# Kernel optimization log

Measured on AMD Instinct MI355X. Metric: run time of the kernel, lower is better.

## Reference

```python
import jax, jax.numpy as jnp
import numpy as np

H = 1536      # hidden_size
V = 128       # input_size == output_size (char vocab)
ML = 128      # MAX_LENGTH
SOS = 0


def setup_inputs() -> dict:
    key = jax.random.key(0)
    ks = jax.random.split(key, 16)
    s = 1.0 / np.sqrt(H)
    f = lambda k, shp: jax.random.uniform(k, shp, jnp.float32, -s, s)
    return {
        "input_tensor": jax.random.randint(ks[0], (64,), 0, V),
        "max_length": ML,
        # encoder params
        "emb_enc": f(ks[1], (V, H)),
        "enc_Wih": f(ks[2], (3 * H, H)),
        "enc_Whh": f(ks[3], (3 * H, H)),
        "enc_bih": f(ks[4], (3 * H,)),
        "enc_bhh": f(ks[5], (3 * H,)),
        # decoder params
        "emb_dec": f(ks[6], (V, H)),
        "attn_W": f(ks[7], (ML + 1, 2 * H)),
        "attn_b": f(ks[8], (ML + 1,)),
        "comb_W": f(ks[9], (H, 2 * H)),
        "comb_b": f(ks[10], (H,)),
        "dec_Wih": f(ks[11], (3 * H, H)),
        "dec_Whh": f(ks[12], (3 * H, H)),
        "dec_bih": f(ks[13], (3 * H,)),
        "dec_bhh": f(ks[14], (3 * H,)),
        "out_W": f(ks[15], (V, H)),
        "out_b": jnp.zeros((V,), jnp.float32),
    }


def gru_step(x, h, Wih, Whh, bih, bhh):
    # PyTorch GRUCell math
    gi = Wih @ x + bih
    gh = Whh @ h + bhh
    i_r, i_z, i_n = jnp.split(gi, 3)
    h_r, h_z, h_n = jnp.split(gh, 3)
    r = jax.nn.sigmoid(i_r + h_r)
    z = jax.nn.sigmoid(i_z + h_z)
    n = jnp.tanh(i_n + r * h_n)
    return (1.0 - z) * n + z * h


def reference(input_tensor, max_length, emb_enc, enc_Wih, enc_Whh, enc_bih,
              enc_bhh, emb_dec, attn_W, attn_b, comb_W, comb_b, dec_Wih,
              dec_Whh, dec_bih, dec_bhh, out_W, out_b):
    L = input_tensor.shape[0]

    # ---- encoder: sequential GRU over input tokens ----
    def enc_step(h, tok):
        h = gru_step(emb_enc[tok], h, enc_Wih, enc_Whh, enc_bih, enc_bhh)
        return h, h
    h0 = jnp.zeros((H,), emb_enc.dtype)
    enc_h, enc_outs = jax.lax.scan(enc_step, h0, input_tensor)  # (L, H)
    encoder_outputs = jnp.zeros((max_length + 1, H), emb_enc.dtype).at[:L].set(enc_outs)

    # ---- attention decoder: greedy decode for max_length steps ----
    def dec_step(carry, _):
        h, tok = carry
        emb = emb_dec[tok]                                   # (H,)
        attn_logits = attn_W @ jnp.concatenate([emb, h]) + attn_b
        attn_w = jax.nn.softmax(attn_logits)                 # (ML+1,)
        context = attn_w @ encoder_outputs                   # (H,)
        x = jax.nn.relu(comb_W @ jnp.concatenate([emb, context]) + comb_b)
        h = gru_step(x, h, dec_Wih, dec_Whh, dec_bih, dec_bhh)
        logp = jax.nn.log_softmax(out_W @ h + out_b)         # (V,)
        nxt = jnp.argmax(logp).astype(tok.dtype)
        return (h, nxt), (logp, nxt)

    tok0 = jnp.asarray(SOS, input_tensor.dtype)
    _, (logps, tokens) = jax.lax.scan(dec_step, (enc_h, tok0), None,
                                      length=max_length)
    return logps, tokens  # (ML, V) log-probs, (ML,) greedy token ids
```

## Files before the change

### kernel.cpp

```cpp
#include <hip/hip_runtime.h>
#include <math.h>

#define H     1536
#define H3    4608
#define V     128
#define ML    128
#define MLP1  129
#define LEN   64
#define NBLK  256
#define NTHR  384
#define WPB   6
#define NWAVE (NBLK*WPB)
#define ACC_N    260
#define ACC_ROWS 8
#define ACC_STEP (ACC_ROWS*ACC_N)
#define TA_STRIDE 132

#define SCALEF     1099511627776.0f
#define INV_SCALED 9.094947017729282379150390625e-13

#define CH_ENC 0
#define CH_EX  1
#define CH_EH  2
#define CH_EA  3

#define OFF_BAR 0
#define OFF_CNT 4096
#define OFF_ACC 8192
#define MEMSET_BYTES 2154752
#define OFF_HS  2154752
#define OFF_XS  2941184
#define OFF_XE  3727616
#define OFF_GI  4120832
#define OFF_EO  5300480
#define OFF_M   5693696
#define OFF_TA  6086912
#define OFF_TC  6154496
#define OFF_CT  6940928
#define WS_END  8538368

__device__ __forceinline__ void uc_stf(float* p, float v){
  __hip_atomic_store(p, v, __ATOMIC_RELAXED, __HIP_MEMORY_SCOPE_AGENT);
}
__device__ __forceinline__ unsigned uc_ldu(const unsigned* p){
  return __hip_atomic_load(p, __ATOMIC_RELAXED, __HIP_MEMORY_SCOPE_AGENT);
}
__device__ __forceinline__ void uc_stu64(unsigned long long* p, unsigned long long v){
  __hip_atomic_store(p, v, __ATOMIC_RELAXED, __HIP_MEMORY_SCOPE_AGENT);
}

__device__ __forceinline__ void bump(unsigned* cnt, int ch, int b){
  __hip_atomic_fetch_add(cnt + (ch*16 + (b>>4))*16, 1u,
                         __ATOMIC_RELAXED, __HIP_MEMORY_SCOPE_AGENT);
}
__device__ __forceinline__ void waitline(const unsigned* cnt, int ch, int tid,
                                         unsigned target){
  if(tid < 16){
    const unsigned* line = cnt + (ch*16 + tid)*16;
    while(uc_ldu(line) < target) __builtin_amdgcn_s_sleep(1);
  }
}

__device__ __forceinline__ float wred(float v){
  #pragma unroll
  for(int s=32;s>0;s>>=1) v += __shfl_xor(v, s, 64);
  return v;
}

__device__ __forceinline__ void load6(const float* p, int lane, float4 r[6]){
  const float4* q = (const float4*)p;
  #pragma unroll
  for(int c=0;c<6;c++) r[c] = q[c*64+lane];
}
__device__ __forceinline__ float dot4(const float4 a, const float4 b){
  return a.x*b.x + a.y*b.y + a.z*b.z + a.w*b.w;
}
__device__ __forceinline__ float dot6(const float4 a[6], const float4 b[6]){
  float s=0.f;
  #pragma unroll
  for(int c=0;c<6;c++) s += dot4(a[c], b[c]);
  return s;
}

__device__ __forceinline__ void gbar(unsigned* bar, int rnd){
  __syncthreads();
  if(threadIdx.x==0){
    unsigned* grp  = bar + 32*(1 + (blockIdx.x >> 4));
    unsigned* root = bar;
    unsigned a = __hip_atomic_fetch_add(grp, 1u, __ATOMIC_RELAXED, __HIP_MEMORY_SCOPE_AGENT);
    if((a & 0xFFFFu) == (unsigned)(16*rnd + 15)){
      unsigned ra = __hip_atomic_fetch_add(root, 1u, __ATOMIC_RELAXED, __HIP_MEMORY_SCOPE_AGENT);
      if(ra == (unsigned)(16*rnd + 15)){
        #pragma unroll
        for(int g=0; g<16; g++)
          __hip_atomic_fetch_add(bar + 32*(1+g), 0x10000u,
                                 __ATOMIC_RELAXED, __HIP_MEMORY_SCOPE_AGENT);
      } else {
        while((uc_ldu(grp) >> 16) < (unsigned)(rnd+1))
          __builtin_amdgcn_s_sleep(1);
      }
    } else {
      while((uc_ldu(grp) >> 16) < (unsigned)(rnd+1))
        __builtin_amdgcn_s_sleep(1);
    }
  }
  __syncthreads();
}

__global__ __launch_bounds__(NTHR, 2)
void seq2seq_kernel(const int* __restrict__ toks,
                    const float* __restrict__ emb_enc,
                    const float* __restrict__ enc_Wih,
                    const float* __restrict__ enc_Whh,
                    const float* __restrict__ enc_bih,
                    const float* __restrict__ enc_bhh,
                    const float* __restrict__ emb_dec,
                    const float* __restrict__ attn_W,
                    const float* __restrict__ attn_b,
                    const float* __restrict__ comb_W,
                    const float* __restrict__ comb_b,
                    const float* __restrict__ dec_Wih,
                    const float* __restrict__ dec_Whh,
                    const float* __restrict__ dec_bih,
                    const float* __restrict__ dec_bhh,
                    const float* __restrict__ out_W,
                    const float* __restrict__ out_b,
                    float* __restrict__ out,
                    char* __restrict__ ws)
{
  const int tid = threadIdx.x, b = blockIdx.x;
  const int lane = tid & 63, w = tid >> 6;
  const int gw = b*WPB + w;
  int rnd = 0;

  unsigned* bar = (unsigned*)ws;
  unsigned* cnt = (unsigned*)(ws + OFF_CNT);
  unsigned long long* accseq = (unsigned long long*)(ws + OFF_ACC);
  float* hseq = (float*)(ws + OFF_HS);
  float* xseq = (float*)(ws + OFF_XS);
  float* Xe = (float*)(ws + OFF_XE);
  float* Gi = (float*)(ws + OFF_GI);
  float* EO = (float*)(ws + OFF_EO);
  float* Mm = (float*)(ws + OFF_M);
  float* tA = (float*)(ws + OFF_TA);
  float* tC = (float*)(ws + OFF_TC);
  float* cT = (float*)(ws + OFF_CT);

  __shared__ float smem[WPB*3*H];
  __shared__ float sh[H];
  __shared__ float sx[H];
  __shared__ float scT[WPB*ACC_N];
  __shared__ float sv[ACC_N];
  __shared__ float shc[8];

  for(int idx = b*NTHR + tid; idx < LEN*H; idx += NBLK*NTHR){
    int t = idx / H, k = idx - t*H;
    uc_stf(&Xe[idx], emb_enc[toks[t]*H + k]);
  }
  for(int idx = b*NTHR + tid; idx < H*257; idx += NBLK*NTHR){
    int i = idx / 257, c = idx - i*257;
    float v = (c < MLP1) ? attn_W[(size_t)c*2*H + H + i]
                         : out_W[(size_t)(c-MLP1)*H + i];
    uc_stf(&cT[(size_t)i*ACC_N + c], v);
  }
  gbar(bar, rnd++);

  {
    int r = b*18 + w*3;
    for(int g=0; g<4; g++){
      __syncthreads();
      for(int idx = tid; idx < 16*384; idx += NTHR)
        ((float4*)smem)[idx] = ((const float4*)Xe)[g*16*384 + idx];
      __syncthreads();
      float4 rv0[6], rv1[6], rv2[6];
      load6(enc_Wih + (size_t)r*H,     lane, rv0);
      load6(enc_Wih + (size_t)(r+1)*H, lane, rv1);
      load6(enc_Wih + (size_t)(r+2)*H, lane, rv2);
      float a0[16], a1[16], a2[16];
      #pragma unroll
      for(int t2=0;t2<16;t2++){ a0[t2]=0.f; a1[t2]=0.f; a2[t2]=0.f; }
      #pragma unroll
      for(int c=0;c<6;c++){
        #pragma unroll
        for(int t2=0;t2<16;t2++){
          float4 x = ((float4*)smem)[t2*384 + c*64 + lane];
          a0[t2] += dot4(rv0[c], x);
          a1[t2] += dot4(rv1[c], x);
          a2[t2] += dot4(rv2[c], x);
        }
      }
      float bi0 = enc_bih[r], bi1 = enc_bih[r+1], bi2 = enc_bih[r+2];
      #pragma unroll
      for(int t2=0;t2<16;t2++){
        float s0 = wred(a0[t2]), s1 = wred(a1[t2]), s2 = wred(a2[t2]);
        if(lane==0){
          uc_stf(&Gi[(size_t)(g*16+t2)*H3 + r    ], s0 + bi0);
          uc_stf(&Gi[(size_t)(g*16+t2)*H3 + r + 1], s1 + bi1);
          uc_stf(&Gi[(size_t)(g*16+t2)*H3 + r + 2], s2 + bi2);
        }
      }
    }
  }
  gbar(bar, rnd++);

  {
    int i = gw;
    float4 rv[6]; load6(comb_W + (size_t)i*2*H, lane, rv);
    for(int g=0; g<8; g++){
      __syncthreads();
      for(int idx = tid; idx < 16*384; idx += NTHR)
        ((float4*)smem)[idx] = ((const float4*)emb_dec)[g*16*384 + idx];
      __syncthreads();
      float a0[16];
      #pragma unroll
      for(int t2=0;t2<16;t2++) a0[t2]=0.f;
      #pragma unroll
      for(int c=0;c<6;c++){
        #pragma unroll
        for(int t2=0;t2<16;t2++){
          float4 x = ((float4*)smem)[t2*384 + c*64 + lane];
          a0[t2] += dot4(rv[c], x);
        }
      }
      #pragma unroll
      for(int t2=0;t2<16;t2++){
        float s = wred(a0[t2]);
        if(lane==0) uc_stf(&tC[(size_t)(g*16+t2)*H + i], s);
      }
    }
  }

  for(int task = gw; task < MLP1*V; task += NWAVE){
    int j = task >> 7, v = task & 127;
    float4 av[6]; load6(attn_W + (size_t)j*2*H, lane, av);
    float4 ev[6]; load6(emb_dec + (size_t)v*H, lane, ev);
    float s = wred(dot6(av, ev));
    if(lane==0) uc_stf(&tA[v*TA_STRIDE + j], s);
  }
  gbar(bar, rnd++);

  for(int idx = tid; idx < 18*384; idx += NTHR){
    int row = idx/384, k4 = idx - row*384;
    int w2 = row/3, gate = row - w2*3;
    ((float4*)smem)[idx] =
      ((const float4*)enc_Whh)[((size_t)gate*H + b*WPB + w2)*384 + k4];
  }
  const int i0 = gw;
  float gi0 = Gi[(size_t)lane*H3 + i0];
  float gi1 = Gi[(size_t)lane*H3 + i0 + H];
  float gi2 = Gi[(size_t)lane*H3 + i0 + 2*H];
  float eb0 = enc_bhh[i0], eb1 = enc_bhh[i0+H], eb2 = enc_bhh[i0+2*H];
  __syncthreads();

  for(int t=0; t<LEN; t++){
    if(t==0){
      float4 z4 = {0.f,0.f,0.f,0.f};
      ((float4*)sh)[tid] = z4;
    } else {
      waitline(cnt, CH_ENC, tid, (unsigned)(16*t));
      __syncthreads();
      ((float4*)sh)[tid] = ((const float4*)(EO + (size_t)(t-1)*H))[tid];
    }
    __syncthreads();
    float4 hv[6]; load6(sh, lane, hv);
    const float hp = sh[i0];
    float s[3];
    #pragma unroll
    for(int g=0; g<3; g++){
      const float4* sr = (const float4*)smem + (w*3+g)*384;
      float t0=0.f;
      #pragma unroll
      for(int c=0;c<6;c++) t0 += dot4(sr[c*64+lane], hv[c]);
      s[g] = wred(t0);
    }
    float ir = __shfl(gi0, t, 64), iz = __shfl(gi1, t, 64), in_ = __shfl(gi2, t, 64);
    if(lane==0){
      float r = 1.f/(1.f+expf(-(ir + s[0] + eb0)));
      float z = 1.f/(1.f+expf(-(iz + s[1] + eb1)));
      float n = tanhf(in_ + r*(s[2] + eb2));
      float hn = (1.f-z)*n + z*hp;
      uc_stf(&EO[(size_t)t*H + i0], hn);
    }
    __syncthreads();
    if(tid==0) bump(cnt, CH_ENC, b);
  }
  waitline(cnt, CH_ENC, tid, (unsigned)(16*LEN));
  __syncthreads();

  {
    int i = gw;
    float4 rv[6]; load6(comb_W + (size_t)i*2*H + H, lane, rv);
    for(int g=0; g<4; g++){
      __syncthreads();
      for(int idx = tid; idx < 16*384; idx += NTHR)
        ((float4*)smem)[idx] = ((const float4*)EO)[g*16*384 + idx];
      __syncthreads();
      float a0[16];
      #pragma unroll
      for(int t2=0;t2<16;t2++) a0[t2]=0.f;
      #pragma unroll
      for(int c=0;c<6;c++){
        #pragma unroll
        for(int t2=0;t2<16;t2++){
          float4 x = ((float4*)smem)[t2*384 + c*64 + lane];
          a0[t2] += dot4(rv[c], x);
        }
      }
      #pragma unroll
      for(int t2=0;t2<16;t2++){
        float s = wred(a0[t2]);
        if(lane==0) uc_stf(&Mm[(size_t)i*64 + g*16 + t2], s);
      }
    }
  }

  if(gw < MLP1){
    int j = gw;
    float4 av[6]; load6(attn_W + (size_t)j*2*H + H, lane, av);
    float4 hv[6]; load6(EO + (size_t)(LEN-1)*H, lane, hv);
    float s = wred(dot6(av, hv));
    if(lane==0)
      uc_stu64(&accseq[j], (unsigned long long)(long long)rintf(s*SCALEF));
  }
  for(int idx = tid; idx < 18*384; idx += NTHR){
    int row = idx/384, k4 = idx - row*384;
    int w2 = row/3, gate = row - w2*3;
    ((float4*)smem)[idx] =
      ((const float4*)dec_Whh)[((size_t)gate*H + b*WPB + w2)*384 + k4];
  }
  for(int idx = tid; idx < WPB*ACC_N; idx += NTHR){
    int w2 = idx / ACC_N, c = idx - w2*ACC_N;
    scT[idx] = cT[(size_t)(b*WPB + w2)*ACC_N + c];
  }
  gbar(bar, rnd++);

  const int i = gw;
  float4 wx0[6], wx1[6], wx2[6];
  load6(dec_Wih + (size_t)i*H,         lane, wx0);
  load6(dec_Wih + ((size_t)H + i)*H,   lane, wx1);
  load6(dec_Wih + ((size_t)2*H + i)*H, lane, wx2);
  const float mreg = Mm[(size_t)i*64 + lane];
  const float ct0 = tC[(size_t)lane*H + i];
  const float ct1 = tC[(size_t)(64+lane)*H + i];
  const float ib0 = dec_bih[i], ib1 = dec_bih[i+H], ib2 = dec_bih[i+2*H];
  const float hb0 = dec_bhh[i], hb1 = dec_bhh[i+H], hb2 = dec_bhh[i+2*H];
  const float cb  = comb_b[i];
  const float ob0 = out_b[lane], ob1 = out_b[64+lane];
  const float ab0 = attn_b[lane], ab1 = attn_b[64+lane], ab2 = attn_b[128];

  for(int t=0; t<ML; t++){
    const unsigned long long* accC = accseq + (size_t)t*ACC_STEP;
    unsigned long long* accA = accseq + (size_t)(t+1)*ACC_STEP;

    if(t==0){
      ((float4*)sh)[tid] = ((const float4*)(EO + (size_t)(LEN-1)*H))[tid];
    } else {
      waitline(cnt, CH_EH, tid, (unsigned)(16*t));
      __syncthreads();
      ((float4*)sh)[tid] = ((const float4*)(hseq + (size_t)(t-1)*H))[tid];
    }
    __syncthreads();

    float4 hv[6]; load6(sh, lane, hv);
    const float hp = sh[i];
    float sWh[3];
    #pragma unroll
    for(int g=0; g<3; g++){
      const float4* sp = (const float4*)smem + (w*3+g)*384;
      float t1=0.f;
      #pragma unroll
      for(int c=0;c<6;c++) t1 += dot4(sp[c*64+lane], hv[c]);
      sWh[g] = wred(t1);
    }

    if(t>0) waitline(cnt, CH_EA, tid, (unsigned)(16*t));
    __syncthreads();
    if(tid < 257){
      long long s = 0;
      #pragma unroll
      for(int r2=0; r2<ACC_ROWS; r2++)
        s += ((const long long*)accC)[r2*ACC_N + tid];
      sv[tid] = (float)((double)s * INV_SCALED);
    }
    __syncthreads();

    float o0 = sv[MLP1+lane]    + ob0;
    float o1 = sv[MLP1+64+lane] + ob1;
    float mv; int mi;
    if(o0 >= o1){ mv=o0; mi=lane; } else { mv=o1; mi=64+lane; }
    #pragma unroll
    for(int sft=32; sft>0; sft>>=1){
      float ov = __shfl_xor(mv, sft, 64);
      int   oi = __shfl_xor(mi, sft, 64);
      if(ov > mv || (ov == mv && oi < mi)){ mv = ov; mi = oi; }
    }
    const int tok = (t==0) ? 0 : mi;

    float v0 = sv[lane]      + tA[tok*TA_STRIDE + lane]      + ab0;
    float v1 = sv[64+lane]   + tA[tok*TA_STRIDE + 64 + lane] + ab1;
    float v2 = (lane==0) ? (sv[128] + tA[tok*TA_STRIDE + 128] + ab2) : -1e30f;
    float m0 = fmaxf(fmaxf(v0, v1), v2);
    #pragma unroll
    for(int sft=32; sft>0; sft>>=1) m0 = fmaxf(m0, __shfl_xor(m0, sft, 64));
    float e0 = expf(v0 - m0);
    float esum = e0 + expf(v1 - m0) + ((lane==0) ? expf(v2 - m0) : 0.f);
    esum = wred(esum);
    const float invd = 1.f/esum;

    {
      float s = wred(mreg * e0);
      float ctv = (tok < 64) ? __shfl(ct0, tok, 64) : __shfl(ct1, tok-64, 64);
      if(lane==0)
        uc_stf(&xseq[(size_t)t*H + i], fmaxf(ctv + s*invd + cb, 0.f));
    }
    __syncthreads();
    if(tid==0) bump(cnt, CH_EX, b);

    waitline(cnt, CH_EX, tid, (unsigned)(16*(t+1)));
    __syncthreads();
    ((float4*)sx)[tid] = ((const float4*)(xseq + (size_t)t*H))[tid];
    __syncthreads();
    float4 xv[6]; load6(sx, lane, xv);
    float t0=0.f, t1=0.f, t2=0.f;
    #pragma unroll
    for(int c=0;c<6;c++){
      t0 += dot4(wx0[c], xv[c]);
      t1 += dot4(wx1[c], xv[c]);
      t2 += dot4(wx2[c], xv[c]);
    }
    float sWx0 = wred(t0), sWx1 = wred(t1), sWx2 = wred(t2);
    if(lane==0){
      float r = 1.f/(1.f+expf(-(sWx0+ib0 + sWh[0]+hb0)));
      float z = 1.f/(1.f+expf(-(sWx1+ib1 + sWh[1]+hb1)));
      float n = tanhf(sWx2+ib2 + r*(sWh[2]+hb2));
      float hn = (1.f-z)*n + z*hp;
      uc_stf(&hseq[(size_t)t*H + i], hn);
      shc[w] = hn;
    }
    __syncthreads();
    if(tid==0) bump(cnt, CH_EH, b);

    if(tid < 257){
      float s = 0.f;
      #pragma unroll
      for(int w2=0; w2<WPB; w2++)
        s += scT[w2*ACC_N + tid] * shc[w2];
      atomicAdd(&accA[(b & (ACC_ROWS-1))*ACC_N + tid],
                (unsigned long long)(long long)rintf(s*SCALEF));
    }
    __syncthreads();
    if(tid==0) bump(cnt, CH_EA, b);
  }

  waitline(cnt, CH_EA, tid, (unsigned)(16*ML));
  __syncthreads();
  if(b < ML && w == 0){
    const unsigned long long* accC = accseq + (size_t)(b+1)*ACC_STEP;
    long long s0 = 0, s1 = 0;
    #pragma unroll
    for(int r2=0; r2<ACC_ROWS; r2++){
      s0 += ((const long long*)accC)[r2*ACC_N + MLP1 + lane];
      s1 += ((const long long*)accC)[r2*ACC_N + MLP1 + 64 + lane];
    }
    float o0 = (float)((double)s0 * INV_SCALED) + ob0;
    float o1 = (float)((double)s1 * INV_SCALED) + ob1;
    float mv; int mi;
    if(o0 >= o1){ mv=o0; mi=lane; } else { mv=o1; mi=64+lane; }
    #pragma unroll
    for(int sft=32; sft>0; sft>>=1){
      float ov = __shfl_xor(mv, sft, 64);
      int   oi = __shfl_xor(mi, sft, 64);
      if(ov > mv || (ov == mv && oi < mi)){ mv = ov; mi = oi; }
    }
    float e0 = expf(o0-mv) + expf(o1-mv);
    float ss = wred(e0);
    float lse = mv + logf(ss);
    out[(size_t)b*V + lane]      = o0 - lse;
    out[(size_t)b*V + 64 + lane] = o1 - lse;
    if(lane==0) out[(size_t)ML*V + b] = (float)mi;
  }
}

extern "C" void kernel_launch(void* const* d_in, const int* in_sizes, int n_in,
                              void* d_out, int out_size, void* d_ws, size_t ws_size,
                              hipStream_t stream){
  (void)in_sizes; (void)n_in; (void)out_size; (void)ws_size;
  const int*   toks    = (const int*)  d_in[0];
  const float* emb_enc = (const float*)d_in[2];
  const float* enc_Wih = (const float*)d_in[3];
  const float* enc_Whh = (const float*)d_in[4];
  const float* enc_bih = (const float*)d_in[5];
  const float* enc_bhh = (const float*)d_in[6];
  const float* emb_dec = (const float*)d_in[7];
  const float* attn_W  = (const float*)d_in[8];
  const float* attn_b  = (const float*)d_in[9];
  const float* comb_W  = (const float*)d_in[10];
  const float* comb_b  = (const float*)d_in[11];
  const float* dec_Wih = (const float*)d_in[12];
  const float* dec_Whh = (const float*)d_in[13];
  const float* dec_bih = (const float*)d_in[14];
  const float* dec_bhh = (const float*)d_in[15];
  const float* out_W   = (const float*)d_in[16];
  const float* out_b   = (const float*)d_in[17];
  float* outp = (float*)d_out;
  char*  ws   = (char*)d_ws;

  hipMemsetAsync(d_ws, 0, MEMSET_BYTES, stream);

  void* args[] = { &toks, &emb_enc, &enc_Wih, &enc_Whh, &enc_bih, &enc_bhh,
                   &emb_dec, &attn_W, &attn_b, &comb_W, &comb_b,
                   &dec_Wih, &dec_Whh, &dec_bih, &dec_bhh, &out_W, &out_b,
                   &outp, &ws };
  hipLaunchCooperativeKernel((void*)seq2seq_kernel, dim3(NBLK), dim3(NTHR),
                             args, 0, stream);
}
```

Measured before the change: 2.040 ms.

## Spread arrival counters over more lines and drop LDS staging of shared vectors

Counter channels now use 32 cache lines with 8 blocks each instead of 16 lines with 16 blocks, lowering atomic contention per line. Waiters poll 32 lines, and the targets are scaled to match. Each wave now loads the hidden state, the x vector and the accumulator sums straight from global memory into registers, instead of staging them through shared memory with extra __syncthreads. This removes block barriers and LDS copies on the serial critical path, at the cost of redundant global/L2 reads per wave and polling more lines.

```diff
diff --git a/kernel.cpp b/kernel.cpp
--- a/kernel.cpp
+++ b/kernel.cpp
@@ -23,21 +23,22 @@
 #define CH_EX  1
 #define CH_EH  2
 #define CH_EA  3
+#define NLINE  32
 
 #define OFF_BAR 0
 #define OFF_CNT 4096
-#define OFF_ACC 8192
-#define MEMSET_BYTES 2154752
-#define OFF_HS  2154752
-#define OFF_XS  2941184
-#define OFF_XE  3727616
-#define OFF_GI  4120832
-#define OFF_EO  5300480
-#define OFF_M   5693696
-#define OFF_TA  6086912
-#define OFF_TC  6154496
-#define OFF_CT  6940928
-#define WS_END  8538368
+#define OFF_ACC 12288
+#define MEMSET_BYTES 2158848
+#define OFF_HS  2158848
+#define OFF_XS  2945280
+#define OFF_XE  3731712
+#define OFF_GI  4124928
+#define OFF_EO  5304576
+#define OFF_M   5697792
+#define OFF_TA  6091008
+#define OFF_TC  6158592
+#define OFF_CT  6945024
+#define WS_END  8542464
 
 __device__ __forceinline__ void uc_stf(float* p, float v){
   __hip_atomic_store(p, v, __ATOMIC_RELAXED, __HIP_MEMORY_SCOPE_AGENT);
@@ -50,13 +51,13 @@
 }
 
 __device__ __forceinline__ void bump(unsigned* cnt, int ch, int b){
-  __hip_atomic_fetch_add(cnt + (ch*16 + (b>>4))*16, 1u,
+  __hip_atomic_fetch_add(cnt + (ch*NLINE + (b>>3))*16, 1u,
                          __ATOMIC_RELAXED, __HIP_MEMORY_SCOPE_AGENT);
 }
 __device__ __forceinline__ void waitline(const unsigned* cnt, int ch, int tid,
                                          unsigned target){
-  if(tid < 16){
-    const unsigned* line = cnt + (ch*16 + tid)*16;
+  if(tid < NLINE){
+    const unsigned* line = cnt + (ch*NLINE + tid)*16;
     while(uc_ldu(line) < target) __builtin_amdgcn_s_sleep(1);
   }
 }
@@ -147,10 +148,7 @@
   float* cT = (float*)(ws + OFF_CT);
 
   __shared__ float smem[WPB*3*H];
-  __shared__ float sh[H];
-  __shared__ float sx[H];
   __shared__ float scT[WPB*ACC_N];
-  __shared__ float sv[ACC_N];
   __shared__ float shc[8];
 
   for(int idx = b*NTHR + tid; idx < LEN*H; idx += NBLK*NTHR){
@@ -253,17 +251,19 @@
   __syncthreads();
 
   for(int t=0; t<LEN; t++){
+    float4 hv[6];
+    float hp;
     if(t==0){
       float4 z4 = {0.f,0.f,0.f,0.f};
-      ((float4*)sh)[tid] = z4;
+      #pragma unroll
+      for(int c=0;c<6;c++) hv[c] = z4;
+      hp = 0.f;
     } else {
-      waitline(cnt, CH_ENC, tid, (unsigned)(16*t));
-      __syncthreads();
-      ((float4*)sh)[tid] = ((const float4*)(EO + (size_t)(t-1)*H))[tid];
-    }
-    __syncthreads();
-    float4 hv[6]; load6(sh, lane, hv);
-    const float hp = sh[i0];
+      waitline(cnt, CH_ENC, tid, (unsigned)(8*t));
+      __syncthreads();
+      load6(EO + (size_t)(t-1)*H, lane, hv);
+      hp = EO[(size_t)(t-1)*H + i0];
+    }
     float s[3];
     #pragma unroll
     for(int g=0; g<3; g++){
@@ -284,7 +284,7 @@
     __syncthreads();
     if(tid==0) bump(cnt, CH_ENC, b);
   }
-  waitline(cnt, CH_ENC, tid, (unsigned)(16*LEN));
+  waitline(cnt, CH_ENC, tid, (unsigned)(8*LEN));
   __syncthreads();
 
   {
@@ -352,17 +352,14 @@
     const unsigned long long* accC = accseq + (size_t)t*ACC_STEP;
     unsigned long long* accA = accseq + (size_t)(t+1)*ACC_STEP;
 
-    if(t==0){
-      ((float4*)sh)[tid] = ((const float4*)(EO + (size_t)(LEN-1)*H))[tid];
-    } else {
-      waitline(cnt, CH_EH, tid, (unsigned)(16*t));
-      __syncthreads();
-      ((float4*)sh)[tid] = ((const float4*)(hseq + (size_t)(t-1)*H))[tid];
-    }
-    __syncthreads();
-
-    float4 hv[6]; load6(sh, lane, hv);
-    const float hp = sh[i];
+    const float* hprev = (t==0) ? (EO + (size_t)(LEN-1)*H) : (hseq + (size_t)(t-1)*H);
+    if(t>0){
+      waitline(cnt, CH_EH, tid, (unsigned)(8*t));
+      __syncthreads();
+    }
+    float4 hv[6]; load6(hprev, lane, hv);
+    const float hp = hprev[i];
+
     float sWh[3];
     #pragma unroll
     for(int g=0; g<3; g++){
@@ -373,19 +370,26 @@
       sWh[g] = wred(t1);
     }
 
-    if(t>0) waitline(cnt, CH_EA, tid, (unsigned)(16*t));
+    if(t>0) waitline(cnt, CH_EA, tid, (unsigned)(8*t));
     __syncthreads();
-    if(tid < 257){
-      long long s = 0;
-      #pragma unroll
-      for(int r2=0; r2<ACC_ROWS; r2++)
-        s += ((const long long*)accC)[r2*ACC_N + tid];
-      sv[tid] = (float)((double)s * INV_SCALED);
-    }
-    __syncthreads();
-
-    float o0 = sv[MLP1+lane]    + ob0;
-    float o1 = sv[MLP1+64+lane] + ob1;
+
+    const long long* aC = (const long long*)accC;
+    long long s0=0, s1=0, ax0=0, ax1=0;
+    #pragma unroll
+    for(int r2=0; r2<ACC_ROWS; r2++){
+      s0  += aC[r2*ACC_N + MLP1 + lane];
+      s1  += aC[r2*ACC_N + MLP1 + 64 + lane];
+      ax0 += aC[r2*ACC_N + lane];
+      ax1 += aC[r2*ACC_N + 64 + lane];
+    }
+    long long ax2 = 0;
+    if(lane==0){
+      #pragma unroll
+      for(int r2=0; r2<ACC_ROWS; r2++) ax2 += aC[r2*ACC_N + 128];
+    }
+
+    float o0 = (float)((double)s0 * INV_SCALED) + ob0;
+    float o1 = (float)((double)s1 * INV_SCALED) + ob1;
     float mv; int mi;
     if(o0 >= o1){ mv=o0; mi=lane; } else { mv=o1; mi=64+lane; }
     #pragma unroll
@@ -396,9 +400,11 @@
     }
     const int tok = (t==0) ? 0 : mi;
 
-    float v0 = sv[lane]      + tA[tok*TA_STRIDE + lane]      + ab0;
-    float v1 = sv[64+lane]   + tA[tok*TA_STRIDE + 64 + lane] + ab1;
-    float v2 = (lane==0) ? (sv[128] + tA[tok*TA_STRIDE + 128] + ab2) : -1e30f;
+    float v0 = (float)((double)ax0 * INV_SCALED) + tA[tok*TA_STRIDE + lane]      + ab0;
+    float v1 = (float)((double)ax1 * INV_SCALED) + tA[tok*TA_STRIDE + 64 + lane] + ab1;
+    float v2 = (lane==0)
+             ? ((float)((double)ax2 * INV_SCALED) + tA[tok*TA_STRIDE + 128] + ab2)
+             : -1e30f;
     float m0 = fmaxf(fmaxf(v0, v1), v2);
     #pragma unroll
     for(int sft=32; sft>0; sft>>=1) m0 = fmaxf(m0, __shfl_xor(m0, sft, 64));
@@ -416,11 +422,9 @@
     __syncthreads();
     if(tid==0) bump(cnt, CH_EX, b);
 
-    waitline(cnt, CH_EX, tid, (unsigned)(16*(t+1)));
+    waitline(cnt, CH_EX, tid, (unsigned)(8*(t+1)));
     __syncthreads();
-    ((float4*)sx)[tid] = ((const float4*)(xseq + (size_t)t*H))[tid];
-    __syncthreads();
-    float4 xv[6]; load6(sx, lane, xv);
+    float4 xv[6]; load6(xseq + (size_t)t*H, lane, xv);
     float t0=0.f, t1=0.f, t2=0.f;
     #pragma unroll
     for(int c=0;c<6;c++){
@@ -452,7 +456,7 @@
     if(tid==0) bump(cnt, CH_EA, b);
   }
 
-  waitline(cnt, CH_EA, tid, (unsigned)(16*ML));
+  waitline(cnt, CH_EA, tid, (unsigned)(8*ML));
   __syncthreads();
   if(b < ML && w == 0){
     const unsigned long long* accC = accseq + (size_t)(b+1)*ACC_STEP;
```

New measurement: 2.155 ms. 1.06x slower.
